# Kernel optimization log

Measured on AMD Instinct MI355X. Metric: run time of the kernel, lower is better.

Reference implementation:

```python
import jax, jax.numpy as jnp
import numpy as np

B, T, D_MODEL = 256, 200, 2048
D_KEY, D_VAL = 128, 128


def setup_inputs() -> dict:
    key = jax.random.key(0)
    k_q, k_mask, k_wq, k_wk, k_wv = jax.random.split(key, 5)
    q = jax.random.normal(k_q, (B, T, D_MODEL), dtype=jnp.float32)
    pad_mask = jax.random.randint(k_mask, (B, 1, T), 0, 2, dtype=jnp.int32)
    # ensure key 0 is never padded so every causal row has >=1 valid key (no NaN softmax)
    pad_mask = pad_mask.at[:, :, 0].set(0)
    s = 1.0 / np.sqrt(D_MODEL)
    Wq = jax.random.normal(k_wq, (D_KEY, D_MODEL), dtype=jnp.float32) * s
    Wk = jax.random.normal(k_wk, (D_KEY, D_MODEL), dtype=jnp.float32) * s
    Wv = jax.random.normal(k_wv, (D_VAL, D_MODEL), dtype=jnp.float32) * s
    return {"q": q, "pad_mask": pad_mask, "Wq": Wq, "Wk": Wk, "Wv": Wv}


def reference(q, pad_mask, Wq, Wk, Wv):
    # self-attention: kv = q
    T_ = q.shape[1]
    C = q.shape[-1]  # note: original scales by d_model, not d_key
    Q = jnp.einsum('btc,kc->btk', q, Wq)   # [B,T,d_key]
    K = jnp.einsum('btc,kc->btk', q, Wk)   # [B,T,d_key]
    V = jnp.einsum('btc,vc->btv', q, Wv)   # [B,T,d_val]
    W = jnp.einsum('bqk,btk->bqt', Q, K) / jnp.sqrt(jnp.asarray(C, q.dtype))  # [B,T,T]
    tril = jnp.tril(jnp.ones((T_, T_), dtype=jnp.bool_))
    neg_inf = jnp.asarray(-jnp.inf, W.dtype)
    W = jnp.where(tril[None, :, :], W, neg_inf)          # causal mask
    W = jnp.where(pad_mask == 1, neg_inf, W)             # padding mask (broadcast [B,1,T])
    W = jax.nn.softmax(W, axis=-1)
    # dropout p=0.0 / eval mode -> identity
    return jnp.einsum('bqt,btv->bqv', W, V)              # [B,T,d_val]
```

## Files before the change

kernel.cpp:

```cpp
#include <hip/hip_runtime.h>

typedef __bf16 bf16x8 __attribute__((ext_vector_type(8)));
typedef __bf16 bf16x4 __attribute__((ext_vector_type(4)));
typedef float  f32x4  __attribute__((ext_vector_type(4)));

#define MFMA16(a,b,c) __builtin_amdgcn_mfma_f32_16x16x32_bf16((a),(b),(c),0,0,0)

constexpr int B_ = 256, T_ = 200, DM = 2048, DK = 128;
constexpr int VT_STRIDE = 208;

constexpr size_t OFF_W = 0;
constexpr size_t OFF_Q = 1572864;
constexpr size_t OFF_K = OFF_Q + 13107200;
constexpr size_t OFF_V = OFF_K + 13107200;

#define GLOAD_LDS16(G, L)                                                     \
  __builtin_amdgcn_global_load_lds(                                           \
      (const __attribute__((address_space(1))) void*)(G),                     \
      (__attribute__((address_space(3))) void*)(L), 16, 0, 0)

__global__ __launch_bounds__(256) void wconv_kernel(const float* __restrict__ Wq,
                                                    const float* __restrict__ Wk,
                                                    const float* __restrict__ Wv,
                                                    __bf16* __restrict__ Wcat) {
  int idx = (blockIdx.x * 256 + threadIdx.x) * 4;
  int sel = idx >> 18;
  const float* base = (sel == 0) ? Wq : (sel == 1) ? Wk : Wv;
  float4 f = *(const float4*)(base + (idx - (sel << 18)));
  bf16x4 o;
  o[0] = (__bf16)f.x; o[1] = (__bf16)f.y; o[2] = (__bf16)f.z; o[3] = (__bf16)f.w;
  *(bf16x4*)(Wcat + idx) = o;
}

__global__ __launch_bounds__(256) void proj_kernel(const float* __restrict__ q,
                                                   const __bf16* __restrict__ Wcat,
                                                   __bf16* __restrict__ Qo,
                                                   __bf16* __restrict__ Ko,
                                                   __bf16* __restrict__ Vt) {
  __shared__ alignas(16) char smem[49152];

  const int tid  = threadIdx.x;
  const int lane = tid & 63;
  const int w    = tid >> 6;
  const int wm   = w >> 1, wn = w & 1;
  const int lhi  = lane >> 4, llo = lane & 15;

  const int d  = blockIdx.x;
  const int jj = (d & 7) * 150 + (d >> 3);
  const int mp = jj / 3, nb = jj - mp * 3;
  const int m0 = mp * 128;
  const int col0 = nb * 128;

  f32x4 acc[4][4];
#pragma unroll
  for (int i = 0; i < 4; ++i)
#pragma unroll
    for (int j = 0; j < 4; ++j) acc[i][j] = {0.f, 0.f, 0.f, 0.f};

  const float* agbase = q + (size_t)(m0 + (tid >> 4)) * DM
                          + (((tid & 15) ^ (tid >> 4)) << 2);
  const __bf16* bgbase = Wcat + (size_t)(col0 + (tid >> 3)) * DM
                              + (((tid & 7) ^ ((tid >> 3) & 7)) << 3);

  constexpr int NK = DM / 64;
  for (int t = 0; t < NK; ++t) {
    const int k0 = t * 64;
#pragma unroll
    for (int r = 0; r < 8; ++r)
      GLOAD_LDS16(agbase + (size_t)r * 16 * DM + k0, smem + tid * 16 + r * 4096);
#pragma unroll
    for (int r = 0; r < 4; ++r)
      GLOAD_LDS16(bgbase + (size_t)r * 32 * DM + k0, smem + 32768 + tid * 16 + r * 4096);
    __syncthreads();

#pragma unroll
    for (int kk = 0; kk < 2; ++kk) {
      bf16x8 af[4];
#pragma unroll
      for (int i = 0; i < 4; ++i) {
        const int row = wm * 64 + i * 16 + llo;
        const int c0 = kk * 8 + lhi * 2;
        f32x4 u = *(const f32x4*)(smem + row * 256 + (((c0 ^ llo) & 15) << 4));
        f32x4 v = *(const f32x4*)(smem + row * 256 + ((((c0 + 1) ^ llo) & 15) << 4));
        af[i][0]=(__bf16)u[0]; af[i][1]=(__bf16)u[1]; af[i][2]=(__bf16)u[2]; af[i][3]=(__bf16)u[3];
        af[i][4]=(__bf16)v[0]; af[i][5]=(__bf16)v[1]; af[i][6]=(__bf16)v[2]; af[i][7]=(__bf16)v[3];
      }
      bf16x8 bfr[4];
#pragma unroll
      for (int j = 0; j < 4; ++j) {
        const int row = wn * 64 + j * 16 + llo;
        const int c = kk * 4 + lhi;
        bfr[j] = *(const bf16x8*)(smem + 32768 + row * 128 + (((c ^ (llo & 7)) & 7) << 4));
      }
#pragma unroll
      for (int i = 0; i < 4; ++i)
#pragma unroll
        for (int j = 0; j < 4; ++j) acc[i][j] = MFMA16(af[i], bfr[j], acc[i][j]);
    }
    if (t + 1 < NK) __syncthreads();
  }

  if (nb == 0) {
#pragma unroll
    for (int i = 0; i < 4; ++i)
#pragma unroll
      for (int r = 0; r < 4; ++r) {
        int row = m0 + wm * 64 + i * 16 + lhi * 4 + r;
#pragma unroll
        for (int j = 0; j < 4; ++j)
          Qo[(size_t)row * DK + wn * 64 + j * 16 + llo] = (__bf16)acc[i][j][r];
      }
  } else if (nb == 1) {
#pragma unroll
    for (int i = 0; i < 4; ++i)
#pragma unroll
      for (int r = 0; r < 4; ++r) {
        int row = m0 + wm * 64 + i * 16 + lhi * 4 + r;
#pragma unroll
        for (int j = 0; j < 4; ++j)
          Ko[(size_t)row * DK + wn * 64 + j * 16 + llo] = (__bf16)acc[i][j][r];
      }
  } else {
#pragma unroll
    for (int i = 0; i < 4; ++i)
#pragma unroll
      for (int r = 0; r < 4; ++r) {
        int row = m0 + wm * 64 + i * 16 + lhi * 4 + r;
        int b = row / 200;
        int t = row - b * 200;
#pragma unroll
        for (int j = 0; j < 4; ++j) {
          int col = wn * 64 + j * 16 + llo;
          Vt[((size_t)b * DK + col) * VT_STRIDE + t] = (__bf16)acc[i][j][r];
        }
      }
  }
}

template <int QB>
__global__ __launch_bounds__(256, 1) void attn_kernel(const __bf16* __restrict__ Qg,
                                                      const __bf16* __restrict__ Kg,
                                                      const __bf16* __restrict__ Vt,
                                                      const int* __restrict__ padm,
                                                      float* __restrict__ out) {
  constexpr int Q0     = QB * 64;
  constexpr int KMAX   = (Q0 + 64 < T_) ? (Q0 + 64) : T_;
  constexpr int KTILES = (KMAX + 15) / 16;
  constexpr int KCC    = (KMAX + 31) / 32;
  constexpr int KT16   = KTILES * 16;
  constexpr int KP     = KCC * 32;
  constexpr int VS     = KP + 8;

  __shared__ __bf16 sK[KT16][136];
  __shared__ __bf16 sV[128][VS];
  __shared__ __bf16 sP[4][16][VS];
  __shared__ float  sMask[KT16];

  const int tid  = threadIdx.x;
  const int lane = tid & 63;
  const int w    = tid >> 6;
  const int b    = blockIdx.x;
  const int lhi  = lane >> 4, llo = lane & 15;

  for (int t = tid; t < KT16; t += 256) {
    float mv = -1e30f;
    if (t < KMAX && padm[b * T_ + t] == 0) mv = 0.0f;
    sMask[t] = mv;
  }
  for (int cid = tid; cid < KT16 * 16; cid += 256) {
    int t = cid >> 4, c = (cid & 15) * 8;
    int tg = (t < T_) ? t : (T_ - 1);
    *(bf16x8*)&sK[t][c] = *(const bf16x8*)(Kg + ((size_t)b * T_ + tg) * DK + c);
  }
  {
    constexpr int NCH = KP / 8;
    for (int cid = tid; cid < 128 * NCH; cid += 256) {
      int v = cid / NCH, t0 = (cid % NCH) * 8;
      bf16x8 val;
      if (t0 < VT_STRIDE) {
        val = *(const bf16x8*)(Vt + ((size_t)b * DK + v) * VT_STRIDE + t0);
      } else {
#pragma unroll
        for (int jz = 0; jz < 8; ++jz) val[jz] = (__bf16)0.0f;
      }
      *(bf16x8*)&sV[v][t0] = val;
    }
  }
  if constexpr (KT16 < KP) {
    constexpr int NC = (KP - KT16) / 8;
    for (int idx = tid; idx < 4 * 16 * NC; idx += 256) {
      int ww = idx / (16 * NC);
      int rem = idx % (16 * NC);
      int row = rem / NC, cc = (rem % NC) * 8;
      bf16x8 z;
#pragma unroll
      for (int jz = 0; jz < 8; ++jz) z[jz] = (__bf16)0.0f;
      *(bf16x8*)&sP[ww][row][KT16 + cc] = z;
    }
  }
  __syncthreads();

  const int q0w = Q0 + w * 16;
  bf16x8 qf[4];
  {
    int qrow = q0w + llo;
    if (qrow > T_ - 1) qrow = T_ - 1;
    const __bf16* qp = Qg + ((size_t)b * T_ + qrow) * DK + lhi * 8;
#pragma unroll
    for (int kk = 0; kk < 4; ++kk) qf[kk] = *(const bf16x8*)(qp + kk * 32);
  }

  float sc[KTILES][4];
  const float scale = 0.022097086912079608f;
#pragma unroll
  for (int tt = 0; tt < KTILES; ++tt) {
    f32x4 s = {0.f, 0.f, 0.f, 0.f};
    const __bf16* kp = &sK[tt * 16 + llo][lhi * 8];
#pragma unroll
    for (int kk = 0; kk < 4; ++kk) {
      bf16x8 kf = *(const bf16x8*)(kp + kk * 32);
      s = MFMA16(qf[kk], kf, s);
    }
    const int t = tt * 16 + llo;
    const float madd = sMask[t];
#pragma unroll
    for (int r = 0; r < 4; ++r) {
      int qq = q0w + lhi * 4 + r;
      float v = fmaf(s[r], scale, madd);
      sc[tt][r] = (t > qq) ? -1e30f : v;
    }
  }

#pragma unroll
  for (int r = 0; r < 4; ++r) {
    float mm = -3e38f;
#pragma unroll
    for (int tt = 0; tt < KTILES; ++tt) mm = fmaxf(mm, sc[tt][r]);
#pragma unroll
    for (int off = 1; off < 16; off <<= 1) mm = fmaxf(mm, __shfl_xor(mm, off));
    float ss = 0.f;
#pragma unroll
    for (int tt = 0; tt < KTILES; ++tt) { float e = __expf(sc[tt][r] - mm); sc[tt][r] = e; ss += e; }
#pragma unroll
    for (int off = 1; off < 16; off <<= 1) ss += __shfl_xor(ss, off);
    float inv = 1.0f / ss;
#pragma unroll
    for (int tt = 0; tt < KTILES; ++tt) sc[tt][r] *= inv;
  }

#pragma unroll
  for (int tt = 0; tt < KTILES; ++tt) {
    int t = tt * 16 + llo;
#pragma unroll
    for (int r = 0; r < 4; ++r) sP[w][lhi * 4 + r][t] = (__bf16)sc[tt][r];
  }
  __syncthreads();

  f32x4 oacc[8];
#pragma unroll
  for (int vt = 0; vt < 8; ++vt) oacc[vt] = {0.f, 0.f, 0.f, 0.f};
#pragma unroll
  for (int kc = 0; kc < KCC; ++kc) {
    bf16x8 pa = *(const bf16x8*)&sP[w][llo][kc * 32 + lhi * 8];
#pragma unroll
    for (int vt = 0; vt < 8; ++vt) {
      bf16x8 vb = *(const bf16x8*)&sV[vt * 16 + llo][kc * 32 + lhi * 8];
      oacc[vt] = MFMA16(pa, vb, oacc[vt]);
    }
  }

#pragma unroll
  for (int vt = 0; vt < 8; ++vt) {
#pragma unroll
    for (int r = 0; r < 4; ++r) {
      int qq = q0w + lhi * 4 + r;
      if (qq < T_) out[((size_t)b * T_ + qq) * DK + vt * 16 + llo] = oacc[vt][r];
    }
  }
}

extern "C" void kernel_launch(void* const* d_in, const int* in_sizes, int n_in,
                              void* d_out, int out_size, void* d_ws, size_t ws_size,
                              hipStream_t stream) {
  const float* q    = (const float*)d_in[0];
  const int*   padm = (const int*)d_in[1];
  const float* Wq   = (const float*)d_in[2];
  const float* Wk   = (const float*)d_in[3];
  const float* Wv   = (const float*)d_in[4];
  float* out        = (float*)d_out;

  char* ws = (char*)d_ws;
  __bf16* Wcat = (__bf16*)(ws + OFF_W);
  __bf16* Qb   = (__bf16*)(ws + OFF_Q);
  __bf16* Kb   = (__bf16*)(ws + OFF_K);
  __bf16* Vtb  = (__bf16*)(ws + OFF_V);

  wconv_kernel<<<768, 256, 0, stream>>>(Wq, Wk, Wv, Wcat);
  proj_kernel<<<1200, 256, 0, stream>>>(q, Wcat, Qb, Kb, Vtb);
  attn_kernel<0><<<256, 256, 0, stream>>>(Qb, Kb, Vtb, padm, out);
  attn_kernel<1><<<256, 256, 0, stream>>>(Qb, Kb, Vtb, padm, out);
  attn_kernel<2><<<256, 256, 0, stream>>>(Qb, Kb, Vtb, padm, out);
  attn_kernel<3><<<256, 256, 0, stream>>>(Qb, Kb, Vtb, padm, out);
}
```

Measured before the change: 244.8 us.

## Software-pipeline projection GEMM with register-staged A and double-buffered LDS

Rewrites the projection GEMM main loop to use a K-step of 32 with double-buffered LDS. The fp32 q tile is now loaded into registers a stage ahead, converted to bf16 once, and stored to LDS. Previously fp32 went straight into LDS and was converted at every fragment read. W tiles still go global-to-LDS asynchronously, with explicit vmcnt/lgkmcnt waits and barriers so loads overlap the MFMAs. This shrinks LDS use and removes redundant conversions, but depends on hand-counted waitcnt values being correct.

```diff
diff --git a/kernel.cpp b/kernel.cpp
--- a/kernel.cpp
+++ b/kernel.cpp
@@ -37,7 +37,7 @@
                                                    __bf16* __restrict__ Qo,
                                                    __bf16* __restrict__ Ko,
                                                    __bf16* __restrict__ Vt) {
-  __shared__ alignas(16) char smem[49152];
+  __shared__ alignas(16) char smem[32768];
 
   const int tid  = threadIdx.x;
   const int lane = tid & 63;
@@ -57,48 +57,109 @@
 #pragma unroll
     for (int j = 0; j < 4; ++j) acc[i][j] = {0.f, 0.f, 0.f, 0.f};
 
-  const float* agbase = q + (size_t)(m0 + (tid >> 4)) * DM
-                          + (((tid & 15) ^ (tid >> 4)) << 2);
-  const __bf16* bgbase = Wcat + (size_t)(col0 + (tid >> 3)) * DM
-                              + (((tid & 7) ^ ((tid >> 3) & 7)) << 3);
-
-  constexpr int NK = DM / 64;
-  for (int t = 0; t < NK; ++t) {
-    const int k0 = t * 64;
-#pragma unroll
-    for (int r = 0; r < 8; ++r)
-      GLOAD_LDS16(agbase + (size_t)r * 16 * DM + k0, smem + tid * 16 + r * 4096);
-#pragma unroll
-    for (int r = 0; r < 4; ++r)
-      GLOAD_LDS16(bgbase + (size_t)r * 32 * DM + k0, smem + 32768 + tid * 16 + r * 4096);
-    __syncthreads();
-
-#pragma unroll
-    for (int kk = 0; kk < 2; ++kk) {
-      bf16x8 af[4];
-#pragma unroll
-      for (int i = 0; i < 4; ++i) {
-        const int row = wm * 64 + i * 16 + llo;
-        const int c0 = kk * 8 + lhi * 2;
-        f32x4 u = *(const f32x4*)(smem + row * 256 + (((c0 ^ llo) & 15) << 4));
-        f32x4 v = *(const f32x4*)(smem + row * 256 + ((((c0 + 1) ^ llo) & 15) << 4));
-        af[i][0]=(__bf16)u[0]; af[i][1]=(__bf16)u[1]; af[i][2]=(__bf16)u[2]; af[i][3]=(__bf16)u[3];
-        af[i][4]=(__bf16)v[0]; af[i][5]=(__bf16)v[1]; af[i][6]=(__bf16)v[2]; af[i][7]=(__bf16)v[3];
-      }
-      bf16x8 bfr[4];
-#pragma unroll
-      for (int j = 0; j < 4; ++j) {
-        const int row = wn * 64 + j * 16 + llo;
-        const int c = kk * 4 + lhi;
-        bfr[j] = *(const bf16x8*)(smem + 32768 + row * 128 + (((c ^ (llo & 7)) & 7) << 4));
-      }
-#pragma unroll
-      for (int i = 0; i < 4; ++i)
-#pragma unroll
-        for (int j = 0; j < 4; ++j) acc[i][j] = MFMA16(af[i], bfr[j], acc[i][j]);
-    }
-    if (t + 1 < NK) __syncthreads();
-  }
+  const int arow = tid >> 1, ahalf = tid & 1;
+  const float* aptr = q + (size_t)(m0 + arow) * DM + ahalf * 16;
+  const int aswz = (tid >> 2) & 3;
+  const int aw0 = arow * 64 + (((ahalf * 2)     ^ aswz) << 4);
+  const int aw1 = arow * 64 + (((ahalf * 2 + 1) ^ aswz) << 4);
+  const __bf16* bgbase = Wcat + (size_t)(col0 + (tid >> 2)) * DM
+                              + (((tid & 3) ^ ((tid >> 3) & 3)) << 3);
+  const int fswz = (llo >> 1) & 3;
+  const int aro  = (wm * 64 + llo) * 64 + ((lhi ^ fswz) << 4);
+  const int bro  = (wn * 64 + llo) * 64 + ((lhi ^ fswz) << 4);
+
+  f32x4 r0a, r0b, r0c, r0d, r1a, r1b, r1c, r1d;
+
+#define A_ISSUE(RA, RB, RC, RD, K0)                                           \
+  { const float* p_ = aptr + (K0);                                            \
+    RA = *(const f32x4*)(p_);      RB = *(const f32x4*)(p_ + 4);              \
+    RC = *(const f32x4*)(p_ + 8);  RD = *(const f32x4*)(p_ + 12); }
+
+#define B_ISSUE(BUFB, K0)                                                     \
+  { char* lb_ = smem + 8192 + (BUFB) * 16384 + tid * 16;                      \
+    GLOAD_LDS16(bgbase + (K0), lb_);                                          \
+    GLOAD_LDS16(bgbase + (size_t)64 * DM + (K0), lb_ + 4096); }
+
+#define A_PUB(RA, RB, RC, RD, BUFB)                                           \
+  { char* la_ = smem + (BUFB) * 16384;                                        \
+    bf16x8 p0, p1;                                                            \
+    p0[0]=(__bf16)RA[0]; p0[1]=(__bf16)RA[1]; p0[2]=(__bf16)RA[2]; p0[3]=(__bf16)RA[3]; \
+    p0[4]=(__bf16)RB[0]; p0[5]=(__bf16)RB[1]; p0[6]=(__bf16)RB[2]; p0[7]=(__bf16)RB[3]; \
+    p1[0]=(__bf16)RC[0]; p1[1]=(__bf16)RC[1]; p1[2]=(__bf16)RC[2]; p1[3]=(__bf16)RC[3]; \
+    p1[4]=(__bf16)RD[0]; p1[5]=(__bf16)RD[1]; p1[6]=(__bf16)RD[2]; p1[7]=(__bf16)RD[3]; \
+    *(bf16x8*)(la_ + aw0) = p0;                                               \
+    *(bf16x8*)(la_ + aw1) = p1; }
+
+#define COMPUTE(BUFB)                                                         \
+  { const char* la_ = smem + (BUFB) * 16384;                                  \
+    const char* lb_ = la_ + 8192;                                             \
+    bf16x8 af[4], bfr[4];                                                     \
+    _Pragma("unroll")                                                         \
+    for (int i = 0; i < 4; ++i) af[i]  = *(const bf16x8*)(la_ + aro + i * 1024); \
+    _Pragma("unroll")                                                         \
+    for (int j = 0; j < 4; ++j) bfr[j] = *(const bf16x8*)(lb_ + bro + j * 1024); \
+    _Pragma("unroll")                                                         \
+    for (int i = 0; i < 4; ++i)                                               \
+      _Pragma("unroll")                                                       \
+      for (int j = 0; j < 4; ++j) acc[i][j] = MFMA16(af[i], bfr[j], acc[i][j]); }
+
+#define VMW(N)  asm volatile("s_waitcnt vmcnt(" #N ")" ::: "memory")
+#define LGKM0() asm volatile("s_waitcnt lgkmcnt(0)" ::: "memory")
+#define BAR()   __builtin_amdgcn_s_barrier()
+
+  constexpr int NK = DM / 32;
+  A_ISSUE(r0a, r0b, r0c, r0d, 0);
+  A_ISSUE(r1a, r1b, r1c, r1d, 32);
+  B_ISSUE(0, 0);
+  A_PUB(r0a, r0b, r0c, r0d, 0);
+  VMW(0);
+  LGKM0();
+  BAR();
+
+  for (int tp = 0; tp < 31; ++tp) {
+    const int t0 = tp * 2;
+    {
+      B_ISSUE(1, (t0 + 1) * 32);
+      A_ISSUE(r0a, r0b, r0c, r0d, (t0 + 2) * 32);
+      VMW(10);
+      BAR();
+      COMPUTE(0);
+      A_PUB(r1a, r1b, r1c, r1d, 1);
+      LGKM0();
+      BAR();
+    }
+    {
+      B_ISSUE(0, (t0 + 2) * 32);
+      A_ISSUE(r1a, r1b, r1c, r1d, (t0 + 3) * 32);
+      VMW(10);
+      BAR();
+      COMPUTE(1);
+      A_PUB(r0a, r0b, r0c, r0d, 0);
+      LGKM0();
+      BAR();
+    }
+  }
+  {
+    B_ISSUE(1, 63 * 32);
+    VMW(6);
+    BAR();
+    COMPUTE(0);
+    A_PUB(r1a, r1b, r1c, r1d, 1);
+    LGKM0();
+    BAR();
+  }
+  {
+    VMW(0);
+    BAR();
+    COMPUTE(1);
+  }
+#undef A_ISSUE
+#undef B_ISSUE
+#undef A_PUB
+#undef COMPUTE
+#undef VMW
+#undef LGKM0
+#undef BAR
 
   if (nb == 0) {
 #pragma unroll
```

After: 279.9 us. 1.14x slower.
